# Optimization experiments

Hardware: AMD Instinct MI355X
Metric: run time of the kernel (lower is better)

Reference implementation:

```python
import jax, jax.numpy as jnp
import numpy as np

D_MODEL = 512
N_HEADS = 8
D_HEAD = D_MODEL // N_HEADS


def setup_inputs() -> dict:
    key = jax.random.key(0)
    ks = jax.random.split(key, 10)
    B, N = 4, 2048
    s = 1.0 / np.sqrt(D_MODEL)
    inp = {
        'x': jax.random.normal(ks[0], (B, N, D_MODEL), jnp.float32),
        'attn_bias': jax.random.normal(ks[1], (B, 1, N, N), jnp.float32),
        'wq': jax.random.normal(ks[2], (D_MODEL, D_MODEL), jnp.float32) * s,
        'bq': jnp.zeros((D_MODEL,), jnp.float32),
        'wk': jax.random.normal(ks[3], (D_MODEL, D_MODEL), jnp.float32) * s,
        'bk': jnp.zeros((D_MODEL,), jnp.float32),
        'wv': jax.random.normal(ks[4], (D_MODEL, D_MODEL), jnp.float32) * s,
        'bv': jnp.zeros((D_MODEL,), jnp.float32),
        'wo': jax.random.normal(ks[5], (D_MODEL, D_MODEL), jnp.float32) * s,
        'bo': jnp.zeros((D_MODEL,), jnp.float32),
    }
    return inp


def reference(x, attn_bias, wq, bq, wk, bk, wv, bv, wo, bo):
    B, N, D = x.shape
    h, dh = N_HEADS, D_HEAD
    # projections; weights stored as (in, out) so y = x @ w + b
    q = (x @ wq + bq).reshape(B, N, h, dh).transpose(0, 2, 1, 3)  # (B,h,N,dh)
    k = (x @ wk + bk).reshape(B, N, h, dh).transpose(0, 2, 1, 3)
    v = (x @ wv + bv).reshape(B, N, h, dh).transpose(0, 2, 1, 3)
    scores = jnp.einsum('bhnd,bhmd->bhnm', q, k) / jnp.sqrt(jnp.float32(dh))
    scores = scores + attn_bias  # broadcast over heads
    attn = jax.nn.softmax(scores, axis=-1)
    out = jnp.einsum('bhnm,bhmd->bhnd', attn, v)
    out = out.transpose(0, 2, 1, 3).reshape(B, N, D)
    return out @ wo + bo
```

## Files before the change

### kernel.cpp

```cpp
#include <hip/hip_runtime.h>
#include <hip/hip_bf16.h>

typedef __bf16 bf16x8 __attribute__((ext_vector_type(8)));
typedef float f32x4 __attribute__((ext_vector_type(4)));
typedef float f32x16 __attribute__((ext_vector_type(16)));
using u16 = unsigned short;
using u32 = unsigned int;

#define LDSS 72

__device__ __forceinline__ u16 f2bf(float f) {
  union { float f; u32 u; } v; v.f = f;
  u32 r = v.u + 0x7fffu + ((v.u >> 16) & 1u);
  return (u16)(r >> 16);
}

__device__ __forceinline__ u32 cvt_pk_bf16(float lo, float hi) {
  u32 r;
  asm("v_cvt_pk_bf16_f32 %0, %1, %2" : "=v"(r) : "v"(lo), "v"(hi));
  return r;
}

__global__ void cast_x_kernel(const float* __restrict__ x, u16* __restrict__ xb) {
  int i = (blockIdx.x * 256 + threadIdx.x) * 8;
  float4 f0 = *(const float4*)&x[i];
  float4 f1 = *(const float4*)&x[i + 4];
  u16 u[8];
  u[0] = f2bf(f0.x); u[1] = f2bf(f0.y); u[2] = f2bf(f0.z); u[3] = f2bf(f0.w);
  u[4] = f2bf(f1.x); u[5] = f2bf(f1.y); u[6] = f2bf(f1.z); u[7] = f2bf(f1.w);
  *(uint4*)&xb[i] = *(uint4*)u;
}

__global__ __launch_bounds__(256) void cast_wT_kernel(
    const float* __restrict__ w0, const float* __restrict__ w1,
    const float* __restrict__ w2, const float* __restrict__ w3,
    u16* __restrict__ t0, u16* __restrict__ t1,
    u16* __restrict__ t2, u16* __restrict__ t3) {
  __shared__ u16 tl[64][72];
  int wi = blockIdx.z;
  const float* w; u16* t;
  if (wi == 0)      { w = w0; t = t0; }
  else if (wi == 1) { w = w1; t = t1; }
  else if (wi == 2) { w = w2; t = t2; }
  else              { w = w3; t = t3; }
  int r0 = blockIdx.x * 64, c0 = blockIdx.y * 64;
  int tid = threadIdx.x;
  int row = tid >> 2, q = tid & 3;
#pragma unroll
  for (int j = 0; j < 4; j++) {
    float4 f = *(const float4*)&w[(r0 + row) * 512 + c0 + q * 16 + j * 4];
    tl[row][q * 16 + j * 4 + 0] = f2bf(f.x);
    tl[row][q * 16 + j * 4 + 1] = f2bf(f.y);
    tl[row][q * 16 + j * 4 + 2] = f2bf(f.z);
    tl[row][q * 16 + j * 4 + 3] = f2bf(f.w);
  }
  __syncthreads();
  int crow = tid >> 2;
  u16 tmp[16];
#pragma unroll
  for (int j = 0; j < 16; j++) tmp[j] = tl[q * 16 + j][crow];
  *(uint4*)&t[(c0 + crow) * 512 + r0 + q * 16]     = *(uint4*)&tmp[0];
  *(uint4*)&t[(c0 + crow) * 512 + r0 + q * 16 + 8] = *(uint4*)&tmp[8];
}

__global__ __launch_bounds__(256) void proj_kernel(
    const u16* __restrict__ xb,
    const u16* __restrict__ wqT, const u16* __restrict__ wkT, const u16* __restrict__ wvT,
    const float* __restrict__ bq, const float* __restrict__ bk, const float* __restrict__ bv,
    u16* __restrict__ Q, u16* __restrict__ K, u16* __restrict__ Vt) {
  __shared__ u16 Alds[64 * LDSS];
  __shared__ u16 Blds[64 * LDSS];
  int which = blockIdx.z;
  const u16* wT; const float* bias; u16* out;
  if (which == 0)      { wT = wqT; bias = bq; out = Q; }
  else if (which == 1) { wT = wkT; bias = bk; out = K; }
  else                 { wT = wvT; bias = bv; out = Vt; }

  int m0 = blockIdx.y * 64;
  int n0 = blockIdx.x * 64;
  int tid = threadIdx.x;
  int lane = tid & 63, w = tid >> 6;
  int wm = w >> 1, wn = w & 1;
  int l15 = lane & 15, l4 = lane >> 4;

  int r0 = tid >> 3, c8 = (tid & 7) * 8;

  uint4 ar0 = *(const uint4*)&xb[(m0 + r0) * 512 + c8];
  uint4 ar1 = *(const uint4*)&xb[(m0 + r0 + 32) * 512 + c8];
  uint4 br0 = *(const uint4*)&wT[(n0 + r0) * 512 + c8];
  uint4 br1 = *(const uint4*)&wT[(n0 + r0 + 32) * 512 + c8];

  f32x4 acc[2][2] = {};
  for (int ks = 0; ks < 8; ks++) {
    __syncthreads();
    *(uint4*)&Alds[r0 * LDSS + c8]        = ar0;
    *(uint4*)&Alds[(r0 + 32) * LDSS + c8] = ar1;
    *(uint4*)&Blds[r0 * LDSS + c8]        = br0;
    *(uint4*)&Blds[(r0 + 32) * LDSS + c8] = br1;
    __syncthreads();
    if (ks < 7) {
      int k0 = (ks + 1) * 64;
      ar0 = *(const uint4*)&xb[(m0 + r0) * 512 + k0 + c8];
      ar1 = *(const uint4*)&xb[(m0 + r0 + 32) * 512 + k0 + c8];
      br0 = *(const uint4*)&wT[(n0 + r0) * 512 + k0 + c8];
      br1 = *(const uint4*)&wT[(n0 + r0 + 32) * 512 + k0 + c8];
    }
#pragma unroll
    for (int kk = 0; kk < 2; kk++) {
      bf16x8 a[2], b[2];
#pragma unroll
      for (int f = 0; f < 2; f++) {
        a[f] = *(const bf16x8*)&Alds[(wm * 32 + f * 16 + l15) * LDSS + kk * 32 + l4 * 8];
        b[f] = *(const bf16x8*)&Blds[(wn * 32 + f * 16 + l15) * LDSS + kk * 32 + l4 * 8];
      }
#pragma unroll
      for (int fm = 0; fm < 2; fm++)
#pragma unroll
        for (int fn = 0; fn < 2; fn++) {
          if (which == 2)
            acc[fm][fn] = __builtin_amdgcn_mfma_f32_16x16x32_bf16(b[fn], a[fm], acc[fm][fn], 0, 0, 0);
          else
            acc[fm][fn] = __builtin_amdgcn_mfma_f32_16x16x32_bf16(a[fm], b[fn], acc[fm][fn], 0, 0, 0);
        }
    }
  }
  int bidx = m0 >> 11;
  int head = n0 >> 6;
  if (which == 2) {
#pragma unroll
    for (int fm = 0; fm < 2; fm++)
#pragma unroll
      for (int fn = 0; fn < 2; fn++)
#pragma unroll
        for (int r = 0; r < 4; r++) {
          int drow = wn * 32 + fn * 16 + l4 * 4 + r;
          int col  = wm * 32 + fm * 16 + l15;
          float vv = acc[fm][fn][r] + bias[n0 + drow];
          out[((size_t)(bidx * 8 + head) * 64 + drow) * 2048 + (m0 & 2047) + col] = f2bf(vv);
        }
  } else {
#pragma unroll
    for (int fm = 0; fm < 2; fm++)
#pragma unroll
      for (int fn = 0; fn < 2; fn++)
#pragma unroll
        for (int r = 0; r < 4; r++) {
          int row = wm * 32 + fm * 16 + l4 * 4 + r;
          int col = wn * 32 + fn * 16 + l15;
          int nrow = (m0 & 2047) + row;
          float vv = acc[fm][fn][r] + bias[n0 + col];
          out[(((size_t)(bidx * 8 + head) * 2048) + nrow) * 64 + col] = f2bf(vv);
        }
  }
}

__global__ __launch_bounds__(128) void attn_kernel(
    const u16* __restrict__ Q, const u16* __restrict__ K, const u16* __restrict__ Vt,
    const float* __restrict__ bias, u16* __restrict__ O) {
  __shared__ u16 Klds[64 * LDSS];
  __shared__ u16 Vtlds[64 * LDSS];

  int qt = blockIdx.x, h = blockIdx.y, b = blockIdx.z;
  int tid = threadIdx.x;
  int lane = tid & 63, w = tid >> 6;
  int l31 = lane & 31, hi = lane >> 5;
  int qrow = qt * 64 + w * 32 + l31;

  const u16* Qbh  = Q  + (size_t)(b * 8 + h) * 2048 * 64;
  const u16* Kbh  = K  + (size_t)(b * 8 + h) * 2048 * 64;
  const u16* Vtbh = Vt + (size_t)(b * 8 + h) * 64 * 2048;
  const float* biasq = bias + (size_t)b * 2048 * 2048 + (size_t)qrow * 2048;

  bf16x8 qf[4];
#pragma unroll
  for (int dk = 0; dk < 4; dk++)
    qf[dk] = *(const bf16x8*)&Qbh[qrow * 64 + dk * 16 + hi * 8];

  f32x16 o[2] = {};
  float mrow = -1e30f, lrow = 0.f;

  int r0 = tid >> 3, c8 = (tid & 7) * 8;

  uint4 kr0 = *(const uint4*)&Kbh[(r0     ) * 64 + c8];
  uint4 kr1 = *(const uint4*)&Kbh[(r0 + 16) * 64 + c8];
  uint4 kr2 = *(const uint4*)&Kbh[(r0 + 32) * 64 + c8];
  uint4 kr3 = *(const uint4*)&Kbh[(r0 + 48) * 64 + c8];
  uint4 vr0 = *(const uint4*)&Vtbh[(r0     ) * 2048 + c8];
  uint4 vr1 = *(const uint4*)&Vtbh[(r0 + 16) * 2048 + c8];
  uint4 vr2 = *(const uint4*)&Vtbh[(r0 + 32) * 2048 + c8];
  uint4 vr3 = *(const uint4*)&Vtbh[(r0 + 48) * 2048 + c8];
  float4 bb[8];
#pragma unroll
  for (int kt = 0; kt < 2; kt++)
#pragma unroll
    for (int g = 0; g < 4; g++)
      bb[kt * 4 + g] = *(const float4*)&biasq[kt * 32 + 8 * g + 4 * hi];

  for (int t = 0; t < 32; t++) {
    __syncthreads();
    *(uint4*)&Klds[(r0     ) * LDSS + c8] = kr0;
    *(uint4*)&Klds[(r0 + 16) * LDSS + c8] = kr1;
    *(uint4*)&Klds[(r0 + 32) * LDSS + c8] = kr2;
    *(uint4*)&Klds[(r0 + 48) * LDSS + c8] = kr3;
    *(uint4*)&Vtlds[(r0     ) * LDSS + c8] = vr0;
    *(uint4*)&Vtlds[(r0 + 16) * LDSS + c8] = vr1;
    *(uint4*)&Vtlds[(r0 + 32) * LDSS + c8] = vr2;
    *(uint4*)&Vtlds[(r0 + 48) * LDSS + c8] = vr3;
    __syncthreads();

    bool pf = (t < 31);
    if (pf) {
      int kb = (t + 1) * 64;
      kr0 = *(const uint4*)&Kbh[(kb + r0     ) * 64 + c8];
      kr1 = *(const uint4*)&Kbh[(kb + r0 + 16) * 64 + c8];
      kr2 = *(const uint4*)&Kbh[(kb + r0 + 32) * 64 + c8];
      kr3 = *(const uint4*)&Kbh[(kb + r0 + 48) * 64 + c8];
      vr0 = *(const uint4*)&Vtbh[(r0     ) * 2048 + kb + c8];
      vr1 = *(const uint4*)&Vtbh[(r0 + 16) * 2048 + kb + c8];
      vr2 = *(const uint4*)&Vtbh[(r0 + 32) * 2048 + kb + c8];
      vr3 = *(const uint4*)&Vtbh[(r0 + 48) * 2048 + kb + c8];
    }

    f32x16 s[2] = {};
    __builtin_amdgcn_s_setprio(1);
#pragma unroll
    for (int dk = 0; dk < 4; dk++) {
      bf16x8 a0 = *(const bf16x8*)&Klds[l31 * LDSS + dk * 16 + hi * 8];
      s[0] = __builtin_amdgcn_mfma_f32_32x32x16_bf16(a0, qf[dk], s[0], 0, 0, 0);
      bf16x8 a1 = *(const bf16x8*)&Klds[(32 + l31) * LDSS + dk * 16 + hi * 8];
      s[1] = __builtin_amdgcn_mfma_f32_32x32x16_bf16(a1, qf[dk], s[1], 0, 0, 0);
    }
    __builtin_amdgcn_s_setprio(0);

    float m = -1e30f;
#pragma unroll
    for (int kt = 0; kt < 2; kt++)
#pragma unroll
      for (int g = 0; g < 4; g++) {
        float4 bv4 = bb[kt * 4 + g];
#pragma unroll
        for (int j = 0; j < 4; j++) {
          float val = s[kt][g * 4 + j] * 0.125f + ((const float*)&bv4)[j];
          s[kt][g * 4 + j] = val;
          m = fmaxf(m, val);
        }
      }
    m = fmaxf(m, __shfl_xor(m, 32));

    if (!__all(m <= mrow + 8.0f)) {
      float mnew = fmaxf(mrow, m);
      float corr = __expf(mrow - mnew);
      mrow = mnew;
      lrow *= corr;
#pragma unroll
      for (int dt = 0; dt < 2; dt++)
#pragma unroll
        for (int i = 0; i < 16; i++) o[dt][i] *= corr;
    }

    u32 c[2][8];
    float sum = 0.f;
#pragma unroll
    for (int kt = 0; kt < 2; kt++)
#pragma unroll
      for (int g = 0; g < 4; g++) {
        float p0 = __expf(s[kt][g * 4 + 0] - mrow);
        float p1 = __expf(s[kt][g * 4 + 1] - mrow);
        float p2 = __expf(s[kt][g * 4 + 2] - mrow);
        float p3 = __expf(s[kt][g * 4 + 3] - mrow);
        sum += (p0 + p1) + (p2 + p3);
        c[kt][2 * g]     = cvt_pk_bf16(p0, p1);
        c[kt][2 * g + 1] = cvt_pk_bf16(p2, p3);
      }
    sum += __shfl_xor(sum, 32);
    lrow += sum;

    u32 dx[2][8];
#pragma unroll
    for (int kt = 0; kt < 2; kt++)
#pragma unroll
      for (int j = 0; j < 8; j++)
        dx[kt][j] = (u32)__shfl_xor((int)c[kt][j], 32);

    if (pf) {
#pragma unroll
      for (int kt = 0; kt < 2; kt++)
#pragma unroll
        for (int g = 0; g < 4; g++)
          bb[kt * 4 + g] = *(const float4*)&biasq[(t + 1) * 64 + kt * 32 + 8 * g + 4 * hi];
    }

    __builtin_amdgcn_s_setprio(1);
#pragma unroll
    for (int kk = 0; kk < 4; kk++) {
      const int kt = kk >> 1, jA = 4 * (kk & 1);
      union { u32 u[4]; bf16x8 v; } pfg;
      pfg.u[0] = hi ? dx[kt][jA + 2] : c[kt][jA];
      pfg.u[1] = hi ? dx[kt][jA + 3] : c[kt][jA + 1];
      pfg.u[2] = hi ? c[kt][jA + 2]  : dx[kt][jA];
      pfg.u[3] = hi ? c[kt][jA + 3]  : dx[kt][jA + 1];
#pragma unroll
      for (int dt = 0; dt < 2; dt++) {
        bf16x8 va = *(const bf16x8*)&Vtlds[(dt * 32 + l31) * LDSS + kk * 16 + hi * 8];
        o[dt] = __builtin_amdgcn_mfma_f32_32x32x16_bf16(va, pfg.v, o[dt], 0, 0, 0);
      }
    }
    __builtin_amdgcn_s_setprio(0);
  }

  float inv = 1.0f / lrow;
  size_t obase = (size_t)(b * 2048 + qrow) * 512 + h * 64;
#pragma unroll
  for (int dt = 0; dt < 2; dt++)
#pragma unroll
    for (int g = 0; g < 4; g++) {
      uint2 pr;
      pr.x = cvt_pk_bf16(o[dt][4 * g + 0] * inv, o[dt][4 * g + 1] * inv);
      pr.y = cvt_pk_bf16(o[dt][4 * g + 2] * inv, o[dt][4 * g + 3] * inv);
      *(uint2*)&O[obase + dt * 32 + 8 * g + 4 * hi] = pr;
    }
}

__global__ __launch_bounds__(256) void outproj_kernel(
    const u16* __restrict__ Ob, const u16* __restrict__ woT,
    const float* __restrict__ bo, float* __restrict__ out) {
  __shared__ u16 Alds[64 * LDSS];
  __shared__ u16 Blds[64 * LDSS];
  int m0 = blockIdx.y * 64;
  int n0 = blockIdx.x * 64;
  int tid = threadIdx.x;
  int lane = tid & 63, w = tid >> 6;
  int wm = w >> 1, wn = w & 1;
  int l15 = lane & 15, l4 = lane >> 4;

  int r0 = tid >> 3, c8 = (tid & 7) * 8;
  uint4 ar0 = *(const uint4*)&Ob[(m0 + r0) * 512 + c8];
  uint4 ar1 = *(const uint4*)&Ob[(m0 + r0 + 32) * 512 + c8];
  uint4 br0 = *(const uint4*)&woT[(n0 + r0) * 512 + c8];
  uint4 br1 = *(const uint4*)&woT[(n0 + r0 + 32) * 512 + c8];

  f32x4 acc[2][2] = {};
  for (int ks = 0; ks < 8; ks++) {
    __syncthreads();
    *(uint4*)&Alds[r0 * LDSS + c8]        = ar0;
    *(uint4*)&Alds[(r0 + 32) * LDSS + c8] = ar1;
    *(uint4*)&Blds[r0 * LDSS + c8]        = br0;
    *(uint4*)&Blds[(r0 + 32) * LDSS + c8] = br1;
    __syncthreads();
    if (ks < 7) {
      int k0 = (ks + 1) * 64;
      ar0 = *(const uint4*)&Ob[(m0 + r0) * 512 + k0 + c8];
      ar1 = *(const uint4*)&Ob[(m0 + r0 + 32) * 512 + k0 + c8];
      br0 = *(const uint4*)&woT[(n0 + r0) * 512 + k0 + c8];
      br1 = *(const uint4*)&woT[(n0 + r0 + 32) * 512 + k0 + c8];
    }
#pragma unroll
    for (int kk = 0; kk < 2; kk++) {
      bf16x8 a[2], bfr[2];
#pragma unroll
      for (int f = 0; f < 2; f++) {
        a[f] = *(const bf16x8*)&Alds[(wm * 32 + f * 16 + l15) * LDSS + kk * 32 + l4 * 8];
        bfr[f] = *(const bf16x8*)&Blds[(wn * 32 + f * 16 + l15) * LDSS + kk * 32 + l4 * 8];
      }
#pragma unroll
      for (int fm = 0; fm < 2; fm++)
#pragma unroll
        for (int fn = 0; fn < 2; fn++)
          acc[fm][fn] = __builtin_amdgcn_mfma_f32_16x16x32_bf16(a[fm], bfr[fn], acc[fm][fn], 0, 0, 0);
    }
  }
#pragma unroll
  for (int fm = 0; fm < 2; fm++)
#pragma unroll
    for (int fn = 0; fn < 2; fn++)
#pragma unroll
      for (int r = 0; r < 4; r++) {
        int row = wm * 32 + fm * 16 + l4 * 4 + r;
        int col = wn * 32 + fn * 16 + l15;
        out[(size_t)(m0 + row) * 512 + n0 + col] = acc[fm][fn][r] + bo[n0 + col];
      }
}

extern "C" void kernel_launch(void* const* d_in, const int* in_sizes, int n_in,
                              void* d_out, int out_size, void* d_ws, size_t ws_size,
                              hipStream_t stream) {
  const float* x    = (const float*)d_in[0];
  const float* bias = (const float*)d_in[1];
  const float* wq   = (const float*)d_in[2];
  const float* bq   = (const float*)d_in[3];
  const float* wk   = (const float*)d_in[4];
  const float* bk   = (const float*)d_in[5];
  const float* wv   = (const float*)d_in[6];
  const float* bv   = (const float*)d_in[7];
  const float* wo   = (const float*)d_in[8];
  const float* bo   = (const float*)d_in[9];
  float* out = (float*)d_out;

  char* ws = (char*)d_ws;
  u16* xb  = (u16*)(ws + 0);
  u16* wqT = (u16*)(ws + 8388608);
  u16* wkT = (u16*)(ws + 8912896);
  u16* wvT = (u16*)(ws + 9437184);
  u16* woT = (u16*)(ws + 9961472);
  u16* Qb  = (u16*)(ws + 10485760);
  u16* Kb  = (u16*)(ws + 18874368);
  u16* VtB = (u16*)(ws + 27262976);
  u16* Ob  = (u16*)(ws + 35651584);

  hipLaunchKernelGGL(cast_x_kernel, dim3(2048), dim3(256), 0, stream, x, xb);
  hipLaunchKernelGGL(cast_wT_kernel, dim3(8, 8, 4), dim3(256), 0, stream,
                     wq, wk, wv, wo, wqT, wkT, wvT, woT);
  hipLaunchKernelGGL(proj_kernel, dim3(8, 128, 3), dim3(256), 0, stream,
                     xb, wqT, wkT, wvT, bq, bk, bv, Qb, Kb, VtB);
  hipLaunchKernelGGL(attn_kernel, dim3(32, 8, 4), dim3(128), 0, stream,
                     Qb, Kb, VtB, bias, Ob);
  hipLaunchKernelGGL(outproj_kernel, dim3(8, 128), dim3(256), 0, stream,
                     Ob, woT, bo, out);
}
```

Measured before the change: 139.7 us.

## Enlarge attention blocks to 128 queries and stage 128 keys per barrier

Result: no change. 139.4 us (-0.2%).

```diff
diff --git a/kernel.cpp b/kernel.cpp
--- a/kernel.cpp
+++ b/kernel.cpp
@@ -154,171 +154,207 @@
   }
 }
 
-__global__ __launch_bounds__(128) void attn_kernel(
+__device__ __forceinline__ void attn_subiter(
+    const u16* __restrict__ Kl, const u16* __restrict__ Vl,
+    float4 bv0, float4 bv1, float4 bv2, float4 bv3,
+    float4 bv4, float4 bv5, float4 bv6, float4 bv7,
+    bf16x8 q0, bf16x8 q1, bf16x8 q2, bf16x8 q3,
+    f32x16& o0, f32x16& o1, float& mrow, float& lrow,
+    int l31, int hi) {
+  bf16x8 qf[4] = {q0, q1, q2, q3};
+  float4 bb[8] = {bv0, bv1, bv2, bv3, bv4, bv5, bv6, bv7};
+
+  f32x16 s[2] = {};
+  __builtin_amdgcn_s_setprio(1);
+#pragma unroll
+  for (int dk = 0; dk < 4; dk++) {
+    bf16x8 a0 = *(const bf16x8*)&Kl[l31 * LDSS + dk * 16 + hi * 8];
+    s[0] = __builtin_amdgcn_mfma_f32_32x32x16_bf16(a0, qf[dk], s[0], 0, 0, 0);
+    bf16x8 a1 = *(const bf16x8*)&Kl[(32 + l31) * LDSS + dk * 16 + hi * 8];
+    s[1] = __builtin_amdgcn_mfma_f32_32x32x16_bf16(a1, qf[dk], s[1], 0, 0, 0);
+  }
+  __builtin_amdgcn_s_setprio(0);
+
+  float m = -1e30f;
+#pragma unroll
+  for (int kt = 0; kt < 2; kt++)
+#pragma unroll
+    for (int g = 0; g < 4; g++) {
+      float4 bv4_ = bb[kt * 4 + g];
+#pragma unroll
+      for (int j = 0; j < 4; j++) {
+        float val = s[kt][g * 4 + j] * 0.125f + ((const float*)&bv4_)[j];
+        s[kt][g * 4 + j] = val;
+        m = fmaxf(m, val);
+      }
+    }
+  m = fmaxf(m, __shfl_xor(m, 32));
+
+  if (!__all(m <= mrow + 8.0f)) {
+    float mnew = fmaxf(mrow, m);
+    float corr = __expf(mrow - mnew);
+    mrow = mnew;
+    lrow *= corr;
+#pragma unroll
+    for (int i = 0; i < 16; i++) { o0[i] *= corr; o1[i] *= corr; }
+  }
+
+  u32 c[2][8];
+  float sum = 0.f;
+#pragma unroll
+  for (int kt = 0; kt < 2; kt++)
+#pragma unroll
+    for (int g = 0; g < 4; g++) {
+      float p0 = __expf(s[kt][g * 4 + 0] - mrow);
+      float p1 = __expf(s[kt][g * 4 + 1] - mrow);
+      float p2 = __expf(s[kt][g * 4 + 2] - mrow);
+      float p3 = __expf(s[kt][g * 4 + 3] - mrow);
+      sum += (p0 + p1) + (p2 + p3);
+      c[kt][2 * g]     = cvt_pk_bf16(p0, p1);
+      c[kt][2 * g + 1] = cvt_pk_bf16(p2, p3);
+    }
+  sum += __shfl_xor(sum, 32);
+  lrow += sum;
+
+  u32 dx[2][8];
+#pragma unroll
+  for (int kt = 0; kt < 2; kt++)
+#pragma unroll
+    for (int j = 0; j < 8; j++)
+      dx[kt][j] = (u32)__shfl_xor((int)c[kt][j], 32);
+
+  __builtin_amdgcn_s_setprio(1);
+#pragma unroll
+  for (int kk = 0; kk < 4; kk++) {
+    const int kt = kk >> 1, jA = 4 * (kk & 1);
+    union { u32 u[4]; bf16x8 v; } pfg;
+    pfg.u[0] = hi ? dx[kt][jA + 2] : c[kt][jA];
+    pfg.u[1] = hi ? dx[kt][jA + 3] : c[kt][jA + 1];
+    pfg.u[2] = hi ? c[kt][jA + 2]  : dx[kt][jA];
+    pfg.u[3] = hi ? c[kt][jA + 3]  : dx[kt][jA + 1];
+    bf16x8 va0 = *(const bf16x8*)&Vl[l31 * LDSS + kk * 16 + hi * 8];
+    o0 = __builtin_amdgcn_mfma_f32_32x32x16_bf16(va0, pfg.v, o0, 0, 0, 0);
+    bf16x8 va1 = *(const bf16x8*)&Vl[(32 + l31) * LDSS + kk * 16 + hi * 8];
+    o1 = __builtin_amdgcn_mfma_f32_32x32x16_bf16(va1, pfg.v, o1, 0, 0, 0);
+  }
+  __builtin_amdgcn_s_setprio(0);
+}
+
+__global__ __launch_bounds__(256, 2) void attn_kernel(
     const u16* __restrict__ Q, const u16* __restrict__ K, const u16* __restrict__ Vt,
     const float* __restrict__ bias, u16* __restrict__ O) {
-  __shared__ u16 Klds[64 * LDSS];
-  __shared__ u16 Vtlds[64 * LDSS];
+  __shared__ u16 Klds[2][64 * LDSS];
+  __shared__ u16 Vtlds[2][64 * LDSS];
 
   int qt = blockIdx.x, h = blockIdx.y, b = blockIdx.z;
   int tid = threadIdx.x;
   int lane = tid & 63, w = tid >> 6;
   int l31 = lane & 31, hi = lane >> 5;
-  int qrow = qt * 64 + w * 32 + l31;
+  int qrow = qt * 128 + w * 32 + l31;
 
   const u16* Qbh  = Q  + (size_t)(b * 8 + h) * 2048 * 64;
   const u16* Kbh  = K  + (size_t)(b * 8 + h) * 2048 * 64;
   const u16* Vtbh = Vt + (size_t)(b * 8 + h) * 64 * 2048;
   const float* biasq = bias + (size_t)b * 2048 * 2048 + (size_t)qrow * 2048;
 
-  bf16x8 qf[4];
-#pragma unroll
-  for (int dk = 0; dk < 4; dk++)
-    qf[dk] = *(const bf16x8*)&Qbh[qrow * 64 + dk * 16 + hi * 8];
-
-  f32x16 o[2] = {};
+  bf16x8 qf0 = *(const bf16x8*)&Qbh[qrow * 64 + 0 * 16 + hi * 8];
+  bf16x8 qf1 = *(const bf16x8*)&Qbh[qrow * 64 + 1 * 16 + hi * 8];
+  bf16x8 qf2 = *(const bf16x8*)&Qbh[qrow * 64 + 2 * 16 + hi * 8];
+  bf16x8 qf3 = *(const bf16x8*)&Qbh[qrow * 64 + 3 * 16 + hi * 8];
+
+  f32x16 o0 = {}, o1 = {};
   float mrow = -1e30f, lrow = 0.f;
 
   int r0 = tid >> 3, c8 = (tid & 7) * 8;
 
-  uint4 kr0 = *(const uint4*)&Kbh[(r0     ) * 64 + c8];
-  uint4 kr1 = *(const uint4*)&Kbh[(r0 + 16) * 64 + c8];
-  uint4 kr2 = *(const uint4*)&Kbh[(r0 + 32) * 64 + c8];
-  uint4 kr3 = *(const uint4*)&Kbh[(r0 + 48) * 64 + c8];
-  uint4 vr0 = *(const uint4*)&Vtbh[(r0     ) * 2048 + c8];
-  uint4 vr1 = *(const uint4*)&Vtbh[(r0 + 16) * 2048 + c8];
-  uint4 vr2 = *(const uint4*)&Vtbh[(r0 + 32) * 2048 + c8];
-  uint4 vr3 = *(const uint4*)&Vtbh[(r0 + 48) * 2048 + c8];
-  float4 bb[8];
-#pragma unroll
-  for (int kt = 0; kt < 2; kt++)
-#pragma unroll
-    for (int g = 0; g < 4; g++)
-      bb[kt * 4 + g] = *(const float4*)&biasq[kt * 32 + 8 * g + 4 * hi];
-
-  for (int t = 0; t < 32; t++) {
-    __syncthreads();
-    *(uint4*)&Klds[(r0     ) * LDSS + c8] = kr0;
-    *(uint4*)&Klds[(r0 + 16) * LDSS + c8] = kr1;
-    *(uint4*)&Klds[(r0 + 32) * LDSS + c8] = kr2;
-    *(uint4*)&Klds[(r0 + 48) * LDSS + c8] = kr3;
-    *(uint4*)&Vtlds[(r0     ) * LDSS + c8] = vr0;
-    *(uint4*)&Vtlds[(r0 + 16) * LDSS + c8] = vr1;
-    *(uint4*)&Vtlds[(r0 + 32) * LDSS + c8] = vr2;
-    *(uint4*)&Vtlds[(r0 + 48) * LDSS + c8] = vr3;
-    __syncthreads();
-
-    bool pf = (t < 31);
+  uint4 kr00 = *(const uint4*)&Kbh[(r0     ) * 64 + c8];
+  uint4 kr01 = *(const uint4*)&Kbh[(r0 + 32) * 64 + c8];
+  uint4 kr10 = *(const uint4*)&Kbh[(64 + r0     ) * 64 + c8];
+  uint4 kr11 = *(const uint4*)&Kbh[(64 + r0 + 32) * 64 + c8];
+  uint4 vr00 = *(const uint4*)&Vtbh[(r0     ) * 2048 + c8];
+  uint4 vr01 = *(const uint4*)&Vtbh[(r0 + 32) * 2048 + c8];
+  uint4 vr10 = *(const uint4*)&Vtbh[(r0     ) * 2048 + 64 + c8];
+  uint4 vr11 = *(const uint4*)&Vtbh[(r0 + 32) * 2048 + 64 + c8];
+
+  float4 bA0 = *(const float4*)&biasq[0 * 32 + 8 * 0 + 4 * hi];
+  float4 bA1 = *(const float4*)&biasq[0 * 32 + 8 * 1 + 4 * hi];
+  float4 bA2 = *(const float4*)&biasq[0 * 32 + 8 * 2 + 4 * hi];
+  float4 bA3 = *(const float4*)&biasq[0 * 32 + 8 * 3 + 4 * hi];
+  float4 bA4 = *(const float4*)&biasq[1 * 32 + 8 * 0 + 4 * hi];
+  float4 bA5 = *(const float4*)&biasq[1 * 32 + 8 * 1 + 4 * hi];
+  float4 bA6 = *(const float4*)&biasq[1 * 32 + 8 * 2 + 4 * hi];
+  float4 bA7 = *(const float4*)&biasq[1 * 32 + 8 * 3 + 4 * hi];
+
+  for (int tt = 0; tt < 16; tt++) {
+    __syncthreads();
+    *(uint4*)&Klds[0][(r0     ) * LDSS + c8] = kr00;
+    *(uint4*)&Klds[0][(r0 + 32) * LDSS + c8] = kr01;
+    *(uint4*)&Klds[1][(r0     ) * LDSS + c8] = kr10;
+    *(uint4*)&Klds[1][(r0 + 32) * LDSS + c8] = kr11;
+    *(uint4*)&Vtlds[0][(r0     ) * LDSS + c8] = vr00;
+    *(uint4*)&Vtlds[0][(r0 + 32) * LDSS + c8] = vr01;
+    *(uint4*)&Vtlds[1][(r0     ) * LDSS + c8] = vr10;
+    *(uint4*)&Vtlds[1][(r0 + 32) * LDSS + c8] = vr11;
+    __syncthreads();
+
+    bool pf = (tt < 15);
     if (pf) {
-      int kb = (t + 1) * 64;
-      kr0 = *(const uint4*)&Kbh[(kb + r0     ) * 64 + c8];
-      kr1 = *(const uint4*)&Kbh[(kb + r0 + 16) * 64 + c8];
-      kr2 = *(const uint4*)&Kbh[(kb + r0 + 32) * 64 + c8];
-      kr3 = *(const uint4*)&Kbh[(kb + r0 + 48) * 64 + c8];
-      vr0 = *(const uint4*)&Vtbh[(r0     ) * 2048 + kb + c8];
-      vr1 = *(const uint4*)&Vtbh[(r0 + 16) * 2048 + kb + c8];
-      vr2 = *(const uint4*)&Vtbh[(r0 + 32) * 2048 + kb + c8];
-      vr3 = *(const uint4*)&Vtbh[(r0 + 48) * 2048 + kb + c8];
-    }
-
-    f32x16 s[2] = {};
-    __builtin_amdgcn_s_setprio(1);
-#pragma unroll
-    for (int dk = 0; dk < 4; dk++) {
-      bf16x8 a0 = *(const bf16x8*)&Klds[l31 * LDSS + dk * 16 + hi * 8];
-      s[0] = __builtin_amdgcn_mfma_f32_32x32x16_bf16(a0, qf[dk], s[0], 0, 0, 0);
-      bf16x8 a1 = *(const bf16x8*)&Klds[(32 + l31) * LDSS + dk * 16 + hi * 8];
-      s[1] = __builtin_amdgcn_mfma_f32_32x32x16_bf16(a1, qf[dk], s[1], 0, 0, 0);
-    }
-    __builtin_amdgcn_s_setprio(0);
-
-    float m = -1e30f;
-#pragma unroll
-    for (int kt = 0; kt < 2; kt++)
-#pragma unroll
-      for (int g = 0; g < 4; g++) {
-        float4 bv4 = bb[kt * 4 + g];
-#pragma unroll
-        for (int j = 0; j < 4; j++) {
-          float val = s[kt][g * 4 + j] * 0.125f + ((const float*)&bv4)[j];
-          s[kt][g * 4 + j] = val;
-          m = fmaxf(m, val);
-        }
-      }
-    m = fmaxf(m, __shfl_xor(m, 32));
-
-    if (!__all(m <= mrow + 8.0f)) {
-      float mnew = fmaxf(mrow, m);
-      float corr = __expf(mrow - mnew);
-      mrow = mnew;
-      lrow *= corr;
-#pragma unroll
-      for (int dt = 0; dt < 2; dt++)
-#pragma unroll
-        for (int i = 0; i < 16; i++) o[dt][i] *= corr;
-    }
-
-    u32 c[2][8];
-    float sum = 0.f;
-#pragma unroll
-    for (int kt = 0; kt < 2; kt++)
-#pragma unroll
-      for (int g = 0; g < 4; g++) {
-        float p0 = __expf(s[kt][g * 4 + 0] - mrow);
-        float p1 = __expf(s[kt][g * 4 + 1] - mrow);
-        float p2 = __expf(s[kt][g * 4 + 2] - mrow);
-        float p3 = __expf(s[kt][g * 4 + 3] - mrow);
-        sum += (p0 + p1) + (p2 + p3);
-        c[kt][2 * g]     = cvt_pk_bf16(p0, p1);
-        c[kt][2 * g + 1] = cvt_pk_bf16(p2, p3);
-      }
-    sum += __shfl_xor(sum, 32);
-    lrow += sum;
-
-    u32 dx[2][8];
-#pragma unroll
-    for (int kt = 0; kt < 2; kt++)
-#pragma unroll
-      for (int j = 0; j < 8; j++)
-        dx[kt][j] = (u32)__shfl_xor((int)c[kt][j], 32);
+      int kb = (tt + 1) * 128;
+      kr00 = *(const uint4*)&Kbh[(kb + r0     ) * 64 + c8];
+      kr01 = *(const uint4*)&Kbh[(kb + r0 + 32) * 64 + c8];
+      kr10 = *(const uint4*)&Kbh[(kb + 64 + r0     ) * 64 + c8];
+      kr11 = *(const uint4*)&Kbh[(kb + 64 + r0 + 32) * 64 + c8];
+      vr00 = *(const uint4*)&Vtbh[(r0     ) * 2048 + kb + c8];
+      vr01 = *(const uint4*)&Vtbh[(r0 + 32) * 2048 + kb + c8];
+      vr10 = *(const uint4*)&Vtbh[(r0     ) * 2048 + kb + 64 + c8];
+      vr11 = *(const uint4*)&Vtbh[(r0 + 32) * 2048 + kb + 64 + c8];
+    }
+
+    int s1b = tt * 128 + 64;
+    float4 bB0 = *(const float4*)&biasq[s1b + 0 * 32 + 8 * 0 + 4 * hi];
+    float4 bB1 = *(const float4*)&biasq[s1b + 0 * 32 + 8 * 1 + 4 * hi];
+    float4 bB2 = *(const float4*)&biasq[s1b + 0 * 32 + 8 * 2 + 4 * hi];
+    float4 bB3 = *(const float4*)&biasq[s1b + 0 * 32 + 8 * 3 + 4 * hi];
+    float4 bB4 = *(const float4*)&biasq[s1b + 1 * 32 + 8 * 0 + 4 * hi];
+    float4 bB5 = *(const float4*)&biasq[s1b + 1 * 32 + 8 * 1 + 4 * hi];
+    float4 bB6 = *(const float4*)&biasq[s1b + 1 * 32 + 8 * 2 + 4 * hi];
+    float4 bB7 = *(const float4*)&biasq[s1b + 1 * 32 + 8 * 3 + 4 * hi];
+
+    attn_subiter(Klds[0], Vtlds[0], bA0, bA1, bA2, bA3, bA4, bA5, bA6, bA7,
+                 qf0, qf1, qf2, qf3, o0, o1, mrow, lrow, l31, hi);
 
     if (pf) {
-#pragma unroll
-      for (int kt = 0; kt < 2; kt++)
-#pragma unroll
-        for (int g = 0; g < 4; g++)
-          bb[kt * 4 + g] = *(const float4*)&biasq[(t + 1) * 64 + kt * 32 + 8 * g + 4 * hi];
-    }
-
-    __builtin_amdgcn_s_setprio(1);
-#pragma unroll
-    for (int kk = 0; kk < 4; kk++) {
-      const int kt = kk >> 1, jA = 4 * (kk & 1);
-      union { u32 u[4]; bf16x8 v; } pfg;
-      pfg.u[0] = hi ? dx[kt][jA + 2] : c[kt][jA];
-      pfg.u[1] = hi ? dx[kt][jA + 3] : c[kt][jA + 1];
-      pfg.u[2] = hi ? c[kt][jA + 2]  : dx[kt][jA];
-      pfg.u[3] = hi ? c[kt][jA + 3]  : dx[kt][jA + 1];
-#pragma unroll
-      for (int dt = 0; dt < 2; dt++) {
-        bf16x8 va = *(const bf16x8*)&Vtlds[(dt * 32 + l31) * LDSS + kk * 16 + hi * 8];
-        o[dt] = __builtin_amdgcn_mfma_f32_32x32x16_bf16(va, pfg.v, o[dt], 0, 0, 0);
-      }
-    }
-    __builtin_amdgcn_s_setprio(0);
+      int s0b = (tt + 1) * 128;
+      bA0 = *(const float4*)&biasq[s0b + 0 * 32 + 8 * 0 + 4 * hi];
+      bA1 = *(const float4*)&biasq[s0b + 0 * 32 + 8 * 1 + 4 * hi];
+      bA2 = *(const float4*)&biasq[s0b + 0 * 32 + 8 * 2 + 4 * hi];
+      bA3 = *(const float4*)&biasq[s0b + 0 * 32 + 8 * 3 + 4 * hi];
+      bA4 = *(const float4*)&biasq[s0b + 1 * 32 + 8 * 0 + 4 * hi];
+      bA5 = *(const float4*)&biasq[s0b + 1 * 32 + 8 * 1 + 4 * hi];
+      bA6 = *(const float4*)&biasq[s0b + 1 * 32 + 8 * 2 + 4 * hi];
+      bA7 = *(const float4*)&biasq[s0b + 1 * 32 + 8 * 3 + 4 * hi];
+    }
+
+    attn_subiter(Klds[1], Vtlds[1], bB0, bB1, bB2, bB3, bB4, bB5, bB6, bB7,
+                 qf0, qf1, qf2, qf3, o0, o1, mrow, lrow, l31, hi);
   }
 
   float inv = 1.0f / lrow;
   size_t obase = (size_t)(b * 2048 + qrow) * 512 + h * 64;
 #pragma unroll
-  for (int dt = 0; dt < 2; dt++)
-#pragma unroll
-    for (int g = 0; g < 4; g++) {
-      uint2 pr;
-      pr.x = cvt_pk_bf16(o[dt][4 * g + 0] * inv, o[dt][4 * g + 1] * inv);
-      pr.y = cvt_pk_bf16(o[dt][4 * g + 2] * inv, o[dt][4 * g + 3] * inv);
-      *(uint2*)&O[obase + dt * 32 + 8 * g + 4 * hi] = pr;
-    }
+  for (int g = 0; g < 4; g++) {
+    uint2 pr;
+    pr.x = cvt_pk_bf16(o0[4 * g + 0] * inv, o0[4 * g + 1] * inv);
+    pr.y = cvt_pk_bf16(o0[4 * g + 2] * inv, o0[4 * g + 3] * inv);
+    *(uint2*)&O[obase + 8 * g + 4 * hi] = pr;
+  }
+#pragma unroll
+  for (int g = 0; g < 4; g++) {
+    uint2 pr;
+    pr.x = cvt_pk_bf16(o1[4 * g + 0] * inv, o1[4 * g + 1] * inv);
+    pr.y = cvt_pk_bf16(o1[4 * g + 2] * inv, o1[4 * g + 3] * inv);
+    *(uint2*)&O[obase + 32 + 8 * g + 4 * hi] = pr;
+  }
 }
 
 __global__ __launch_bounds__(256) void outproj_kernel(
@@ -412,7 +448,7 @@
                      wq, wk, wv, wo, wqT, wkT, wvT, woT);
   hipLaunchKernelGGL(proj_kernel, dim3(8, 128, 3), dim3(256), 0, stream,
                      xb, wqT, wkT, wvT, bq, bk, bv, Qb, Kb, VtB);
-  hipLaunchKernelGGL(attn_kernel, dim3(32, 8, 4), dim3(128), 0, stream,
+  hipLaunchKernelGGL(attn_kernel, dim3(16, 8, 4), dim3(256), 0, stream,
                      Qb, Kb, VtB, bias, Ob);
   hipLaunchKernelGGL(outproj_kernel, dim3(8, 128), dim3(256), 0, stream,
                      Ob, woT, bo, out);
```
